# Kernel optimization log

Measured on AMD Instinct MI355X. Metric: run time of the kernel, lower is better.

The kernel has to match this reference:

```python
import jax, jax.numpy as jnp
import numpy as np
import math

B, S, E = 2, 2048, 1024
H, D = 16, 64
LAMBDA_INIT = 0.8
GN_EPS = 1e-5


def setup_inputs() -> dict:
    key = jax.random.key(0)
    ks = jax.random.split(key, 12)
    s = 0.02
    inputs = jax.random.normal(ks[0], (B, S, E), jnp.float32)
    attention_mask = jnp.ones((B, S), jnp.float32)
    token_indices = jnp.sort(jax.random.randint(ks[1], (B, S), 0, S), axis=-1)
    Wq = jax.random.normal(ks[2], (2 * H * D, E), jnp.float32) * s
    Wk = jax.random.normal(ks[3], (2 * H * D, E), jnp.float32) * s
    Wv = jax.random.normal(ks[4], (H * D, E), jnp.float32) * s
    Wo = jax.random.normal(ks[5], (E, H * D), jnp.float32) * s
    lam_q1 = jax.random.normal(ks[6], (D,), jnp.float32) * 0.1
    lam_q2 = jax.random.normal(ks[7], (D,), jnp.float32) * 0.1
    lam_k1 = jax.random.normal(ks[8], (D,), jnp.float32) * 0.1
    lam_k2 = jax.random.normal(ks[9], (D,), jnp.float32) * 0.1
    gn_w = jnp.ones((H * D,), jnp.float32)
    gn_b = jnp.zeros((H * D,), jnp.float32)
    return dict(inputs=inputs, attention_mask=attention_mask, token_indices=token_indices,
                Wq=Wq, Wk=Wk, Wv=Wv, Wo=Wo,
                lam_q1=lam_q1, lam_q2=lam_q2, lam_k1=lam_k1, lam_k2=lam_k2,
                gn_w=gn_w, gn_b=gn_b)


def reference(inputs, attention_mask, token_indices, Wq, Wk, Wv, Wo,
              lam_q1, lam_q2, lam_k1, lam_k2, gn_w, gn_b):
    b, s, e = inputs.shape
    # projections: q,k have doubled head dim (differential), v is standard
    q = (inputs @ Wq.T).reshape(b, s, H, 2 * D).transpose(0, 2, 1, 3)  # [B,H,S,2D]
    k = (inputs @ Wk.T).reshape(b, s, H, 2 * D).transpose(0, 2, 1, 3)
    v = (inputs @ Wv.T).reshape(b, s, H, D).transpose(0, 2, 1, 3)      # [B,H,S,D]
    Q1, Q2 = q[..., :D], q[..., D:]
    K1, K2 = k[..., :D], k[..., D:]
    scale = 1.0 / math.sqrt(D)
    s1 = jnp.einsum('bhqd,bhkd->bhqk', Q1, K1) * scale
    s2 = jnp.einsum('bhqd,bhkd->bhqk', Q2, K2) * scale
    # ALiBi bias: slopes[h] * (pos_q - pos_k), subtracted
    slopes = 2.0 ** (-8.0 * jnp.arange(1, H + 1, dtype=jnp.float32) / H)
    pos = token_indices.astype(jnp.float32)                            # [B,S]
    pos_diff = pos[:, :, None] - pos[:, None, :]                       # [B,S,S]
    bias = slopes[None, :, None, None] * pos_diff[:, None, :, :]       # [B,H,S,S]
    # causal + padding masks
    causal = jnp.triu(jnp.full((s, s), -1e9, jnp.float32), 1)[None, None]
    pad = (1.0 - attention_mask)[:, None, None, :] * -1e9
    s1 = s1 - bias + causal + pad
    s2 = s2 - bias + causal + pad
    w1 = jax.nn.softmax(s1, axis=-1)
    w2 = jax.nn.softmax(s2, axis=-1)
    lam = jnp.exp(jnp.dot(lam_q1, lam_k1)) - jnp.exp(jnp.dot(lam_q2, lam_k2)) + LAMBDA_INIT
    w = w1 - lam * w2
    out = jnp.einsum('bhqk,bhkd->bhqd', w, v)                          # [B,H,S,D]
    # GroupNorm(num_groups=H, num_channels=H*D) over channels-first layout [B,C,S]
    x = out.transpose(0, 2, 1, 3).reshape(b, s, H * D).transpose(0, 2, 1)  # [B,C,S]
    xg = x.reshape(b, H, D * s)
    mean = xg.mean(axis=-1, keepdims=True)
    var = xg.var(axis=-1, keepdims=True)
    xn = ((xg - mean) / jnp.sqrt(var + GN_EPS)).reshape(b, H * D, s)
    xn = xn * gn_w[None, :, None] + gn_b[None, :, None]
    xn = xn * (1.0 - LAMBDA_INIT)
    attn = xn.transpose(0, 2, 1)                                       # [B,S,H*D]
    return attn @ Wo.T
```

## Files before the change

### kernel.cpp

```cpp
#include <hip/hip_runtime.h>
#include <hip/hip_bf16.h>

typedef __hip_bfloat16 bf16;
typedef float f32x4 __attribute__((ext_vector_type(4)));
typedef float fvec4 __attribute__((ext_vector_type(4)));
typedef short s16x8 __attribute__((ext_vector_type(8)));

#define NB_B 2
#define NB_S 2048
#define NB_E 1024
#define NB_H 16
#define NB_D 64

typedef const __attribute__((address_space(1))) void* GPTR;
typedef __attribute__((address_space(3))) void* LPTR;

__device__ __forceinline__ void gld16(const void* g, void* l) {
  __builtin_amdgcn_global_load_lds((GPTR)g, (LPTR)l, 16, 0, 0);
}

__device__ __forceinline__ s16x8 ld8(const bf16* p) { return *(const s16x8*)p; }

__device__ __forceinline__ f32x4 MFMA(s16x8 a, s16x8 b, f32x4 c) {
  return __builtin_amdgcn_mfma_f32_16x16x32_bf16(a, b, c, 0, 0, 0);
}

struct __align__(8) bf16x4 { bf16 a, b, c, d; };

__global__ void cvt_kernel(const float* __restrict__ in, bf16* __restrict__ out, int n4) {
  int i = blockIdx.x * blockDim.x + threadIdx.x;
  if (i >= n4) return;
  fvec4 v = ((const fvec4*)in)[i];
  bf16x4 o = { bf16(v.x), bf16(v.y), bf16(v.z), bf16(v.w) };
  ((bf16x4*)out)[i] = o;
}

__global__ void cvtw_kernel(const float* __restrict__ wq, const float* __restrict__ wk,
                            const float* __restrict__ wv, const float* __restrict__ wo,
                            bf16* __restrict__ oq, bf16* __restrict__ ok,
                            bf16* __restrict__ ov, bf16* __restrict__ oo) {
  int i = blockIdx.x * 256 + threadIdx.x;
  const float* src; bf16* dst; int off;
  if (i < 524288)       { src = wq; dst = oq; off = i; }
  else if (i < 1048576) { src = wk; dst = ok; off = i - 524288; }
  else if (i < 1310720) { src = wv; dst = ov; off = i - 1048576; }
  else                  { src = wo; dst = oo; off = i - 1310720; }
  fvec4 v = ((const fvec4*)src)[off];
  bf16x4 o = { bf16(v.x), bf16(v.y), bf16(v.z), bf16(v.w) };
  ((bf16x4*)dst)[off] = o;
}

__global__ void lam_kernel(const float* lq1, const float* lq2,
                           const float* lk1, const float* lk2, float* out) {
  int l = threadIdx.x;
  float d1 = lq1[l] * lk1[l];
  float d2 = lq2[l] * lk2[l];
#pragma unroll
  for (int o = 32; o; o >>= 1) { d1 += __shfl_xor(d1, o); d2 += __shfl_xor(d2, o); }
  if (l == 0) out[0] = expf(d1) - expf(d2) + 0.8f;
}

__global__ void combo_kernel(const int* __restrict__ tok, const float* __restrict__ amask,
                             float* __restrict__ combo) {
  int i = blockIdx.x * 256 + threadIdx.x;
  int hh = i >> 12, bs = i & 4095;
  float slopeL = exp2f(-0.5f * (float)(hh + 1)) * 1.44269504088896340736f;
  combo[i] = slopeL * (float)tok[bs] + (amask[bs] - 1.f) * 1.44269504e9f;
}

template <int EPI>
__global__ __launch_bounds__(256) void gemm_bt(const bf16* __restrict__ A,
                                               const bf16* __restrict__ Bw,
                                               bf16* __restrict__ Ob,
                                               bf16* __restrict__ Ob2,
                                               bf16* __restrict__ Ob3,
                                               float* __restrict__ Of,
                                               int Kd, float oscale) {
  __shared__ bf16 As[2][128 * 32];
  __shared__ bf16 Bs[2][128 * 32];
  const int tid = threadIdx.x;
  const int lane = tid & 63;
  const int fr = lane & 15, fq = lane >> 4;
  const int wave = tid >> 6;
  const int wr = (wave >> 1) * 64, wc = (wave & 1) * 64;
  const size_t m0 = (size_t)blockIdx.x * 128, n0 = (size_t)blockIdx.y * 128;

  f32x4 acc[4][4];
#pragma unroll
  for (int i = 0; i < 4; i++)
#pragma unroll
    for (int j = 0; j < 4; j++) acc[i][j] = f32x4{0.f, 0.f, 0.f, 0.f};

  const int ca = tid, cb = tid + 256;
  const bf16* ga0 = A + (m0 + (ca >> 2)) * Kd + (ca & 3) * 8;
  const bf16* ga1 = A + (m0 + (cb >> 2)) * Kd + (cb & 3) * 8;
  const bf16* gb0 = Bw + (n0 + (ca >> 2)) * Kd + (ca & 3) * 8;
  const bf16* gb1 = Bw + (n0 + (cb >> 2)) * Kd + (cb & 3) * 8;

  gld16(ga0, &As[0][ca * 8]);
  gld16(ga1, &As[0][cb * 8]);
  gld16(gb0, &Bs[0][ca * 8]);
  gld16(gb1, &Bs[0][cb * 8]);
  __syncthreads();

  const int NKT = Kd >> 5;
  for (int kti = 0; kti < NKT; ++kti) {
    const int cur = kti & 1;
    if (kti + 1 < NKT) {
      const int kt = (kti + 1) << 5;
      gld16(ga0 + kt, &As[cur ^ 1][ca * 8]);
      gld16(ga1 + kt, &As[cur ^ 1][cb * 8]);
      gld16(gb0 + kt, &Bs[cur ^ 1][ca * 8]);
      gld16(gb1 + kt, &Bs[cur ^ 1][cb * 8]);
    }
    s16x8 af[4], bfv[4];
#pragma unroll
    for (int mi = 0; mi < 4; mi++) af[mi] = ld8(&As[cur][(wr + mi * 16 + fr) * 32 + fq * 8]);
#pragma unroll
    for (int ni = 0; ni < 4; ni++) bfv[ni] = ld8(&Bs[cur][(wc + ni * 16 + fr) * 32 + fq * 8]);
#pragma unroll
    for (int mi = 0; mi < 4; mi++)
#pragma unroll
      for (int ni = 0; ni < 4; ni++)
        acc[mi][ni] = MFMA(af[mi], bfv[ni], acc[mi][ni]);
    __syncthreads();
  }

  bf16* dst = Ob;
  size_t nsub = 0;
  float osc = oscale;
  bool isV = false;
  if constexpr (EPI == 0) {
    if (n0 >= 4096)      { dst = Ob3; nsub = 4096; osc = 1.0f; isV = true; }
    else if (n0 >= 2048) { dst = Ob2; nsub = 2048; osc = 1.0f; }
  }

#pragma unroll
  for (int mi = 0; mi < 4; mi++)
#pragma unroll
    for (int ni = 0; ni < 4; ni++)
#pragma unroll
      for (int i = 0; i < 4; i++) {
        size_t m = m0 + wr + mi * 16 + fq * 4 + i;
        size_t n = n0 + wc + ni * 16 + fr;
        if constexpr (EPI == 0) {
          float v = acc[mi][ni][i] * osc;
          size_t nn = n - nsub;
          size_t b = m >> 11, s = m & 2047;
          if (!isV) {
            size_t h = nn >> 7, dd = nn & 127;
            dst[((b * NB_H + h) * NB_S + s) * 128 + dd] = bf16(v);
          } else {
            size_t h = nn >> 6, d = nn & 63;
            dst[((b * NB_H + h) * NB_D + d) * NB_S + s] = bf16(v);
          }
        } else {
          Of[m * 1024 + n] = acc[mi][ni][i] * oscale;
        }
      }
}

__global__ __launch_bounds__(512, 2) void attn_kernel(
    const bf16* __restrict__ Q, const bf16* __restrict__ Kk, const bf16* __restrict__ Vt,
    const int* __restrict__ tok, const float* __restrict__ combo,
    const float* __restrict__ lamp, float* __restrict__ X) {
  __shared__ bf16 Ks[2][2][4096];
  __shared__ bf16 Vs[2][4096];
  __shared__ bf16 Ps[8][1024];

  const int tid = threadIdx.x, lane = tid & 63, wave = tid >> 6;
  const int fr = lane & 15, fq = lane >> 4;
  const int id = blockIdx.x;
  const int w = id >> 3;
  const int bh = (id & 7) * 4 + (w & 3);
  const int qj = 15 - (w >> 2);
  const int b = bh >> 4, h = bh & 15;

  const float lam = lamp[0];
  const float slopeL = exp2f(-0.5f * (float)(h + 1)) * 1.44269504088896340736f;
  const float* comboH = combo + ((size_t)h * NB_B + b) * NB_S;

  const bf16* Kbase = Kk + (size_t)bh * NB_S * 128;
  const bf16* Vbase = Vt + (size_t)bh * NB_D * NB_S;

  const bf16* gK[2]; int lK[2];
#pragma unroll
  for (int i = 0; i < 2; i++) {
    int c = tid + i * 512, set = c >> 9, cc = c & 511;
    int row = cc >> 3, col8 = cc & 7, sc = col8 ^ (row & 7);
    gK[i] = Kbase + (size_t)row * 128 + set * 64 + sc * 8;
    lK[i] = set * 4096 + cc * 8;
  }
  const bf16* gV; int lV;
  {
    int c = tid;
    int row = c >> 3, col8 = c & 7, sc = col8 ^ (row & 7);
    gV = Vbase + (size_t)row * NB_S + sc * 8;
    lV = c * 8;
  }

  const int q0 = qj * 128;
  const int qw = q0 + wave * 16;
  const int ntiles = 2 * qj + 2;

  const bf16* qrow = Q + ((size_t)bh * NB_S + qw + fr) * 128;
  s16x8 q1[2], q2[2];
  q1[0] = ld8(qrow + fq * 8);       q1[1] = ld8(qrow + 32 + fq * 8);
  q2[0] = ld8(qrow + 64 + fq * 8);  q2[1] = ld8(qrow + 96 + fq * 8);

  const int qg = qw + fr;
  const float pq = slopeL * (float)tok[b * NB_S + qg];

  float m1 = -1e30f, m2 = -1e30f, l1 = 0.f, l2 = 0.f;
  f32x4 acc1[4], acc2[4];
#pragma unroll
  for (int nt = 0; nt < 4; nt++) { acc1[nt] = f32x4{0.f,0.f,0.f,0.f}; acc2[nt] = f32x4{0.f,0.f,0.f,0.f}; }

#pragma unroll
  for (int i = 0; i < 2; i++) gld16(gK[i], &Ks[0][0][0] + lK[i]);
  gld16(gV, &Vs[0][0] + lV);
  __syncthreads();

  for (int t = 0; t < ntiles; ++t) {
    const int cur = t & 1;
    const int kv0 = t * 64;
    if (t + 1 < ntiles) {
#pragma unroll
      for (int i = 0; i < 2; i++)
        gld16(gK[i] + (size_t)(kv0 + 64) * 128, &Ks[cur ^ 1][0][0] + lK[i]);
      gld16(gV + (size_t)(kv0 + 64), &Vs[cur ^ 1][0] + lV);
    }

    const bool active = (kv0 <= qw + 15);
    if (active) {
      fvec4 cmbv[4];
#pragma unroll
      for (int nt = 0; nt < 4; nt++)
        cmbv[nt] = *(const fvec4*)(comboH + kv0 + nt * 16 + fq * 4);

      f32x4 c1[4], c2[4];
#pragma unroll
      for (int nt = 0; nt < 4; nt++) { c1[nt] = f32x4{0.f,0.f,0.f,0.f}; c2[nt] = f32x4{0.f,0.f,0.f,0.f}; }
#pragma unroll
      for (int nt = 0; nt < 4; nt++) {
        const int krow = nt * 16 + fr;
#pragma unroll
        for (int kk = 0; kk < 2; kk++) {
          const int sch = ((kk * 4 + fq) ^ (krow & 7)) * 8;
          c1[nt] = MFMA(ld8(&Ks[cur][0][krow * 64 + sch]), q1[kk], c1[nt]);
          c2[nt] = MFMA(ld8(&Ks[cur][1][krow * 64 + sch]), q2[kk], c2[nt]);
        }
      }

      float sv1[4][4], sv2[4][4];
#pragma unroll
      for (int nt = 0; nt < 4; nt++)
#pragma unroll
        for (int i = 0; i < 4; i++) {
          const float biasv = cmbv[nt][i] - pq;
          sv1[nt][i] = c1[nt][i] + biasv;
          sv2[nt][i] = c2[nt][i] + biasv;
        }
      if (kv0 + 63 > qw) {
#pragma unroll
        for (int nt = 0; nt < 4; nt++)
#pragma unroll
          for (int i = 0; i < 4; i++)
            if (kv0 + nt * 16 + fq * 4 + i > qg) { sv1[nt][i] = -1e30f; sv2[nt][i] = -1e30f; }
      }

      s16x8 vf[4][2];
#pragma unroll
      for (int nt = 0; nt < 4; nt++) {
        const int vrow = nt * 16 + fr;
#pragma unroll
        for (int kk = 0; kk < 2; kk++)
          vf[nt][kk] = ld8(&Vs[cur][vrow * 64 + (((kk * 4 + fq) ^ (vrow & 7)) << 3)]);
      }

      {
        float pm = fmaxf(fmaxf(fmaxf(sv1[0][0], sv1[0][1]), fmaxf(sv1[0][2], sv1[0][3])),
                         fmaxf(fmaxf(sv1[1][0], sv1[1][1]), fmaxf(sv1[1][2], sv1[1][3])));
        pm = fmaxf(pm, fmaxf(fmaxf(fmaxf(sv1[2][0], sv1[2][1]), fmaxf(sv1[2][2], sv1[2][3])),
                             fmaxf(fmaxf(sv1[3][0], sv1[3][1]), fmaxf(sv1[3][2], sv1[3][3]))));
        pm = fmaxf(pm, __shfl_xor(pm, 16));
        pm = fmaxf(pm, __shfl_xor(pm, 32));
        if (__any(pm > m1 + 8.f)) {
          const float nm = fmaxf(m1, pm);
          const float cor = exp2f(m1 - nm);
          m1 = nm; l1 *= cor;
#pragma unroll
          for (int i = 0; i < 4; i++) {
            const float ci = __shfl(cor, fq * 4 + i);
#pragma unroll
            for (int nt = 0; nt < 4; nt++) acc1[nt][i] *= ci;
          }
        }
        float rs = 0.f;
#pragma unroll
        for (int nt = 0; nt < 4; nt++) {
          const float p0 = exp2f(sv1[nt][0] - m1), p1 = exp2f(sv1[nt][1] - m1);
          const float p2 = exp2f(sv1[nt][2] - m1), p3 = exp2f(sv1[nt][3] - m1);
          rs += (p0 + p1) + (p2 + p3);
          bf16x4 pk = { bf16(p0), bf16(p1), bf16(p2), bf16(p3) };
          *(bf16x4*)&Ps[wave][fr * 64 + ((((nt * 4 + fq) ^ ((fr & 7) << 1))) << 2)] = pk;
        }
        rs += __shfl_xor(rs, 16);
        rs += __shfl_xor(rs, 32);
        l1 += rs;
#pragma unroll
        for (int kk = 0; kk < 2; kk++) {
          const s16x8 pa = ld8(&Ps[wave][fr * 64 + (((kk * 8 + fq * 2) ^ ((fr & 7) << 1)) << 2)]);
#pragma unroll
          for (int nt = 0; nt < 4; nt++) acc1[nt] = MFMA(pa, vf[nt][kk], acc1[nt]);
        }
      }
      {
        float pm = fmaxf(fmaxf(fmaxf(sv2[0][0], sv2[0][1]), fmaxf(sv2[0][2], sv2[0][3])),
                         fmaxf(fmaxf(sv2[1][0], sv2[1][1]), fmaxf(sv2[1][2], sv2[1][3])));
        pm = fmaxf(pm, fmaxf(fmaxf(fmaxf(sv2[2][0], sv2[2][1]), fmaxf(sv2[2][2], sv2[2][3])),
                             fmaxf(fmaxf(sv2[3][0], sv2[3][1]), fmaxf(sv2[3][2], sv2[3][3]))));
        pm = fmaxf(pm, __shfl_xor(pm, 16));
        pm = fmaxf(pm, __shfl_xor(pm, 32));
        if (__any(pm > m2 + 8.f)) {
          const float nm = fmaxf(m2, pm);
          const float cor = exp2f(m2 - nm);
          m2 = nm; l2 *= cor;
#pragma unroll
          for (int i = 0; i < 4; i++) {
            const float ci = __shfl(cor, fq * 4 + i);
#pragma unroll
            for (int nt = 0; nt < 4; nt++) acc2[nt][i] *= ci;
          }
        }
        float rs = 0.f;
#pragma unroll
        for (int nt = 0; nt < 4; nt++) {
          const float p0 = exp2f(sv2[nt][0] - m2), p1 = exp2f(sv2[nt][1] - m2);
          const float p2 = exp2f(sv2[nt][2] - m2), p3 = exp2f(sv2[nt][3] - m2);
          rs += (p0 + p1) + (p2 + p3);
          bf16x4 pk = { bf16(p0), bf16(p1), bf16(p2), bf16(p3) };
          *(bf16x4*)&Ps[wave][fr * 64 + ((((nt * 4 + fq) ^ ((fr & 7) << 1))) << 2)] = pk;
        }
        rs += __shfl_xor(rs, 16);
        rs += __shfl_xor(rs, 32);
        l2 += rs;
#pragma unroll
        for (int kk = 0; kk < 2; kk++) {
          const s16x8 pa = ld8(&Ps[wave][fr * 64 + (((kk * 8 + fq * 2) ^ ((fr & 7) << 1)) << 2)]);
#pragma unroll
          for (int nt = 0; nt < 4; nt++) acc2[nt] = MFMA(pa, vf[nt][kk], acc2[nt]);
        }
      }
    }

    __syncthreads();
  }

  const float r1 = 1.f / l1, r2 = lam / l2;
  float r1b[4], r2b[4];
#pragma unroll
  for (int i = 0; i < 4; i++) {
    r1b[i] = __shfl(r1, fq * 4 + i);
    r2b[i] = __shfl(r2, fq * 4 + i);
  }
#pragma unroll
  for (int nt = 0; nt < 4; nt++)
#pragma unroll
    for (int i = 0; i < 4; i++) {
      X[((size_t)bh * NB_S + qw + fq * 4 + i) * NB_D + nt * 16 + fr] =
          acc1[nt][i] * r1b[i] - acc2[nt][i] * r2b[i];
    }
}

__global__ __launch_bounds__(256) void gn_part(const float* __restrict__ X, float* __restrict__ part) {
  const int blk = blockIdx.x;
  const int bh = blk >> 3, seg = blk & 7;
  const float* xp = X + (size_t)bh * 131072 + (size_t)seg * 16384;
  float s = 0.f, s2 = 0.f;
  for (int i = threadIdx.x; i < 4096; i += 256) {
    fvec4 v = ((const fvec4*)xp)[i];
    s += v.x + v.y + v.z + v.w;
    s2 += v.x * v.x + v.y * v.y + v.z * v.z + v.w * v.w;
  }
#pragma unroll
  for (int o = 32; o; o >>= 1) { s += __shfl_xor(s, o); s2 += __shfl_xor(s2, o); }
  __shared__ float rs[4], rq[4];
  const int wv = threadIdx.x >> 6, ln = threadIdx.x & 63;
  if (ln == 0) { rs[wv] = s; rq[wv] = s2; }
  __syncthreads();
  if (threadIdx.x == 0) {
    part[blk * 2] = rs[0] + rs[1] + rs[2] + rs[3];
    part[blk * 2 + 1] = rq[0] + rq[1] + rq[2] + rq[3];
  }
}

__global__ __launch_bounds__(256) void gn_apply(const float* __restrict__ X,
                                                const float* __restrict__ part,
                                                const float* __restrict__ gw,
                                                const float* __restrict__ gb,
                                                bf16* __restrict__ Xn) {
  const int blk = blockIdx.x, bh = blk >> 3, seg = blk & 7;
  const int b = bh >> 4, h = bh & 15;
  float s = 0.f, s2 = 0.f;
#pragma unroll
  for (int i = 0; i < 8; i++) { s += part[(bh * 8 + i) * 2]; s2 += part[(bh * 8 + i) * 2 + 1]; }
  const float mean = s * (1.f / 131072.f);
  const float var = s2 * (1.f / 131072.f) - mean * mean;
  const float rstd = rsqrtf(var + 1e-5f) * 0.2f;
  const float* xp = X + (size_t)bh * 131072 + (size_t)seg * 16384;
  for (int i = threadIdx.x; i < 4096; i += 256) {
    fvec4 v = ((const fvec4*)xp)[i];
    const int e = seg * 16384 + i * 4;
    const int srow = e >> 6, d = e & 63;
    const int c = h * 64 + d;
    bf16x4 o = { bf16((v.x - mean) * rstd * gw[c]     + 0.2f * gb[c]),
                 bf16((v.y - mean) * rstd * gw[c + 1] + 0.2f * gb[c + 1]),
                 bf16((v.z - mean) * rstd * gw[c + 2] + 0.2f * gb[c + 2]),
                 bf16((v.w - mean) * rstd * gw[c + 3] + 0.2f * gb[c + 3]) };
    *(bf16x4*)(Xn + ((size_t)b * NB_S + srow) * 1024 + c) = o;
  }
}

extern "C" void kernel_launch(void* const* d_in, const int* in_sizes, int n_in,
                              void* d_out, int out_size, void* d_ws, size_t ws_size,
                              hipStream_t stream) {
  const float* inputs = (const float*)d_in[0];
  const float* amask  = (const float*)d_in[1];
  const int*   tok    = (const int*)d_in[2];
  const float* Wq = (const float*)d_in[3];
  const float* Wk = (const float*)d_in[4];
  const float* Wv = (const float*)d_in[5];
  const float* Wo = (const float*)d_in[6];
  const float* lq1 = (const float*)d_in[7];
  const float* lq2 = (const float*)d_in[8];
  const float* lk1 = (const float*)d_in[9];
  const float* lk2 = (const float*)d_in[10];
  const float* gw = (const float*)d_in[11];
  const float* gb = (const float*)d_in[12];
  float* out = (float*)d_out;
  char* ws = (char*)d_ws;

  bf16* Xbf = (bf16*)(ws + 0);
  bf16* Wqb = (bf16*)(ws + 8388608);
  bf16* Wkb = (bf16*)(ws + 12582912);
  bf16* Wvb = (bf16*)(ws + 16777216);
  float* X  = (float*)(ws + 0);
  float* combo = (float*)(ws + 16777216);
  bf16* Qb  = (bf16*)(ws + 18874368);
  bf16* Xn  = (bf16*)(ws + 18874368);
  bf16* Kb  = (bf16*)(ws + 35651584);
  bf16* Vtb = (bf16*)(ws + 52428800);
  bf16* Wob = (bf16*)(ws + 60817408);
  float* lam = (float*)(ws + 62914560);
  float* gnp = (float*)(ws + 62914816);

  const float QSCALE = 0.125f * 1.44269504088896340736f;

  cvt_kernel<<<4096, 256, 0, stream>>>(inputs, Xbf, 1048576);
  cvtw_kernel<<<6144, 256, 0, stream>>>(Wq, Wk, Wv, Wo, Wqb, Wkb, Wvb, Wob);
  lam_kernel<<<1, 64, 0, stream>>>(lq1, lq2, lk1, lk2, lam);

  gemm_bt<0><<<dim3(32, 40), 256, 0, stream>>>(Xbf, Wqb, Qb, Kb, Vtb, nullptr, 1024, QSCALE);

  combo_kernel<<<256, 256, 0, stream>>>(tok, amask, combo);

  attn_kernel<<<512, 512, 0, stream>>>(Qb, Kb, Vtb, tok, combo, lam, X);

  gn_part<<<256, 256, 0, stream>>>(X, gnp);
  gn_apply<<<256, 256, 0, stream>>>(X, gnp, gw, gb, Xn);

  gemm_bt<2><<<dim3(32, 8), 256, 0, stream>>>(Xn, Wob, nullptr, nullptr, nullptr, out, 1024, 1.0f);
}
```

Baseline: 224.8 us.

## Fuse prep kernels, fold GroupNorm stats into attention, compute row sums via MFMA

Merges the input/weight conversion and lambda kernels into one launch. The attention kernel now writes its output in bf16, accumulates the GroupNorm sum and sum-of-squares with atomics, and drops the separate gn_part pass. Softmax row sums are computed with an extra MFMA against a ones vector instead of shuffles, and s_setprio hints are placed around the MFMA blocks. gn_apply reads bf16 with vectorized 8-wide accesses. This trades some precision (bf16 intermediate, bf16-rounded probabilities used in the row sums) and float atomics for fewer launches and less memory traffic.

```diff
diff --git a/kernel.cpp b/kernel.cpp
--- a/kernel.cpp
+++ b/kernel.cpp
@@ -27,37 +27,41 @@
 
 struct __align__(8) bf16x4 { bf16 a, b, c, d; };
 
-__global__ void cvt_kernel(const float* __restrict__ in, bf16* __restrict__ out, int n4) {
-  int i = blockIdx.x * blockDim.x + threadIdx.x;
-  if (i >= n4) return;
-  fvec4 v = ((const fvec4*)in)[i];
-  bf16x4 o = { bf16(v.x), bf16(v.y), bf16(v.z), bf16(v.w) };
-  ((bf16x4*)out)[i] = o;
-}
-
-__global__ void cvtw_kernel(const float* __restrict__ wq, const float* __restrict__ wk,
+__global__ void prep_kernel(const float* __restrict__ inputs,
+                            const float* __restrict__ wq, const float* __restrict__ wk,
                             const float* __restrict__ wv, const float* __restrict__ wo,
+                            const float* __restrict__ lq1, const float* __restrict__ lq2,
+                            const float* __restrict__ lk1, const float* __restrict__ lk2,
+                            bf16* __restrict__ xbf,
                             bf16* __restrict__ oq, bf16* __restrict__ ok,
-                            bf16* __restrict__ ov, bf16* __restrict__ oo) {
-  int i = blockIdx.x * 256 + threadIdx.x;
-  const float* src; bf16* dst; int off;
-  if (i < 524288)       { src = wq; dst = oq; off = i; }
-  else if (i < 1048576) { src = wk; dst = ok; off = i - 524288; }
-  else if (i < 1310720) { src = wv; dst = ov; off = i - 1048576; }
-  else                  { src = wo; dst = oo; off = i - 1310720; }
-  fvec4 v = ((const fvec4*)src)[off];
-  bf16x4 o = { bf16(v.x), bf16(v.y), bf16(v.z), bf16(v.w) };
-  ((bf16x4*)dst)[off] = o;
-}
-
-__global__ void lam_kernel(const float* lq1, const float* lq2,
-                           const float* lk1, const float* lk2, float* out) {
-  int l = threadIdx.x;
-  float d1 = lq1[l] * lk1[l];
-  float d2 = lq2[l] * lk2[l];
-#pragma unroll
-  for (int o = 32; o; o >>= 1) { d1 += __shfl_xor(d1, o); d2 += __shfl_xor(d2, o); }
-  if (l == 0) out[0] = expf(d1) - expf(d2) + 0.8f;
+                            bf16* __restrict__ ov, bf16* __restrict__ oo,
+                            float* __restrict__ lamo) {
+  const int blk = blockIdx.x;
+  if (blk < 4096) {
+    int i = blk * 256 + threadIdx.x;
+    fvec4 v = ((const fvec4*)inputs)[i];
+    bf16x4 o = { bf16(v.x), bf16(v.y), bf16(v.z), bf16(v.w) };
+    ((bf16x4*)xbf)[i] = o;
+  } else if (blk < 10240) {
+    int i = (blk - 4096) * 256 + threadIdx.x;
+    const float* src; bf16* dst; int off;
+    if (i < 524288)       { src = wq; dst = oq; off = i; }
+    else if (i < 1048576) { src = wk; dst = ok; off = i - 524288; }
+    else if (i < 1310720) { src = wv; dst = ov; off = i - 1048576; }
+    else                  { src = wo; dst = oo; off = i - 1310720; }
+    fvec4 v = ((const fvec4*)src)[off];
+    bf16x4 o = { bf16(v.x), bf16(v.y), bf16(v.z), bf16(v.w) };
+    ((bf16x4*)dst)[off] = o;
+  } else {
+    int l = threadIdx.x;
+    if (l < 64) {
+      float d1 = lq1[l] * lk1[l];
+      float d2 = lq2[l] * lk2[l];
+#pragma unroll
+      for (int o = 32; o; o >>= 1) { d1 += __shfl_xor(d1, o); d2 += __shfl_xor(d2, o); }
+      if (l == 0) lamo[0] = expf(d1) - expf(d2) + 0.8f;
+    }
+  }
 }
 
 __global__ void combo_kernel(const int* __restrict__ tok, const float* __restrict__ amask,
@@ -163,10 +167,11 @@
 __global__ __launch_bounds__(512, 2) void attn_kernel(
     const bf16* __restrict__ Q, const bf16* __restrict__ Kk, const bf16* __restrict__ Vt,
     const int* __restrict__ tok, const float* __restrict__ combo,
-    const float* __restrict__ lamp, float* __restrict__ X) {
+    const float* __restrict__ lamp, bf16* __restrict__ Xb, float* __restrict__ gnp) {
   __shared__ bf16 Ks[2][2][4096];
   __shared__ bf16 Vs[2][4096];
   __shared__ bf16 Ps[8][1024];
+  __shared__ float gs[8][2];
 
   const int tid = threadIdx.x, lane = tid & 63, wave = tid >> 6;
   const int fr = lane & 15, fq = lane >> 4;
@@ -183,6 +188,8 @@
   const bf16* Kbase = Kk + (size_t)bh * NB_S * 128;
   const bf16* Vbase = Vt + (size_t)bh * NB_D * NB_S;
 
+  const s16x8 onesv = { 0x3F80, 0x3F80, 0x3F80, 0x3F80, 0x3F80, 0x3F80, 0x3F80, 0x3F80 };
+
   const bf16* gK[2]; int lK[2];
 #pragma unroll
   for (int i = 0; i < 2; i++) {
@@ -211,8 +218,9 @@
   const int qg = qw + fr;
   const float pq = slopeL * (float)tok[b * NB_S + qg];
 
-  float m1 = -1e30f, m2 = -1e30f, l1 = 0.f, l2 = 0.f;
+  float m1 = -1e30f, m2 = -1e30f;
   f32x4 acc1[4], acc2[4];
+  f32x4 accL1 = f32x4{0.f,0.f,0.f,0.f}, accL2 = f32x4{0.f,0.f,0.f,0.f};
 #pragma unroll
   for (int nt = 0; nt < 4; nt++) { acc1[nt] = f32x4{0.f,0.f,0.f,0.f}; acc2[nt] = f32x4{0.f,0.f,0.f,0.f}; }
 
@@ -241,6 +249,7 @@
       f32x4 c1[4], c2[4];
 #pragma unroll
       for (int nt = 0; nt < 4; nt++) { c1[nt] = f32x4{0.f,0.f,0.f,0.f}; c2[nt] = f32x4{0.f,0.f,0.f,0.f}; }
+      __builtin_amdgcn_s_setprio(1);
 #pragma unroll
       for (int nt = 0; nt < 4; nt++) {
         const int krow = nt * 16 + fr;
@@ -251,6 +260,7 @@
           c2[nt] = MFMA(ld8(&Ks[cur][1][krow * 64 + sch]), q2[kk], c2[nt]);
         }
       }
+      __builtin_amdgcn_s_setprio(0);
 
       float sv1[4][4], sv2[4][4];
 #pragma unroll
@@ -288,32 +298,30 @@
         if (__any(pm > m1 + 8.f)) {
           const float nm = fmaxf(m1, pm);
           const float cor = exp2f(m1 - nm);
-          m1 = nm; l1 *= cor;
+          m1 = nm;
 #pragma unroll
           for (int i = 0; i < 4; i++) {
             const float ci = __shfl(cor, fq * 4 + i);
+            accL1[i] *= ci;
 #pragma unroll
             for (int nt = 0; nt < 4; nt++) acc1[nt][i] *= ci;
           }
         }
-        float rs = 0.f;
 #pragma unroll
         for (int nt = 0; nt < 4; nt++) {
-          const float p0 = exp2f(sv1[nt][0] - m1), p1 = exp2f(sv1[nt][1] - m1);
-          const float p2 = exp2f(sv1[nt][2] - m1), p3 = exp2f(sv1[nt][3] - m1);
-          rs += (p0 + p1) + (p2 + p3);
-          bf16x4 pk = { bf16(p0), bf16(p1), bf16(p2), bf16(p3) };
+          bf16x4 pk = { bf16(exp2f(sv1[nt][0] - m1)), bf16(exp2f(sv1[nt][1] - m1)),
+                        bf16(exp2f(sv1[nt][2] - m1)), bf16(exp2f(sv1[nt][3] - m1)) };
           *(bf16x4*)&Ps[wave][fr * 64 + ((((nt * 4 + fq) ^ ((fr & 7) << 1))) << 2)] = pk;
         }
-        rs += __shfl_xor(rs, 16);
-        rs += __shfl_xor(rs, 32);
-        l1 += rs;
+        __builtin_amdgcn_s_setprio(1);
 #pragma unroll
         for (int kk = 0; kk < 2; kk++) {
           const s16x8 pa = ld8(&Ps[wave][fr * 64 + (((kk * 8 + fq * 2) ^ ((fr & 7) << 1)) << 2)]);
+          accL1 = MFMA(pa, onesv, accL1);
 #pragma unroll
           for (int nt = 0; nt < 4; nt++) acc1[nt] = MFMA(pa, vf[nt][kk], acc1[nt]);
         }
+        __builtin_amdgcn_s_setprio(0);
       }
       {
         float pm = fmaxf(fmaxf(fmaxf(sv2[0][0], sv2[0][1]), fmaxf(sv2[0][2], sv2[0][3])),
@@ -325,100 +333,91 @@
         if (__any(pm > m2 + 8.f)) {
           const float nm = fmaxf(m2, pm);
           const float cor = exp2f(m2 - nm);
-          m2 = nm; l2 *= cor;
+          m2 = nm;
 #pragma unroll
           for (int i = 0; i < 4; i++) {
             const float ci = __shfl(cor, fq * 4 + i);
+            accL2[i] *= ci;
 #pragma unroll
             for (int nt = 0; nt < 4; nt++) acc2[nt][i] *= ci;
           }
         }
-        float rs = 0.f;
 #pragma unroll
         for (int nt = 0; nt < 4; nt++) {
-          const float p0 = exp2f(sv2[nt][0] - m2), p1 = exp2f(sv2[nt][1] - m2);
-          const float p2 = exp2f(sv2[nt][2] - m2), p3 = exp2f(sv2[nt][3] - m2);
-          rs += (p0 + p1) + (p2 + p3);
-          bf16x4 pk = { bf16(p0), bf16(p1), bf16(p2), bf16(p3) };
+          bf16x4 pk = { bf16(exp2f(sv2[nt][0] - m2)), bf16(exp2f(sv2[nt][1] - m2)),
+                        bf16(exp2f(sv2[nt][2] - m2)), bf16(exp2f(sv2[nt][3] - m2)) };
           *(bf16x4*)&Ps[wave][fr * 64 + ((((nt * 4 + fq) ^ ((fr & 7) << 1))) << 2)] = pk;
         }
-        rs += __shfl_xor(rs, 16);
-        rs += __shfl_xor(rs, 32);
-        l2 += rs;
+        __builtin_amdgcn_s_setprio(1);
 #pragma unroll
         for (int kk = 0; kk < 2; kk++) {
           const s16x8 pa = ld8(&Ps[wave][fr * 64 + (((kk * 8 + fq * 2) ^ ((fr & 7) << 1)) << 2)]);
+          accL2 = MFMA(pa, onesv, accL2);
 #pragma unroll
           for (int nt = 0; nt < 4; nt++) acc2[nt] = MFMA(pa, vf[nt][kk], acc2[nt]);
         }
+        __builtin_amdgcn_s_setprio(0);
       }
     }
 
     __syncthreads();
   }
 
-  const float r1 = 1.f / l1, r2 = lam / l2;
   float r1b[4], r2b[4];
 #pragma unroll
-  for (int i = 0; i < 4; i++) {
-    r1b[i] = __shfl(r1, fq * 4 + i);
-    r2b[i] = __shfl(r2, fq * 4 + i);
-  }
+  for (int i = 0; i < 4; i++) { r1b[i] = 1.f / accL1[i]; r2b[i] = lam / accL2[i]; }
+  float s = 0.f, s2 = 0.f;
 #pragma unroll
   for (int nt = 0; nt < 4; nt++)
 #pragma unroll
     for (int i = 0; i < 4; i++) {
-      X[((size_t)bh * NB_S + qw + fq * 4 + i) * NB_D + nt * 16 + fr] =
-          acc1[nt][i] * r1b[i] - acc2[nt][i] * r2b[i];
-    }
-}
-
-__global__ __launch_bounds__(256) void gn_part(const float* __restrict__ X, float* __restrict__ part) {
-  const int blk = blockIdx.x;
-  const int bh = blk >> 3, seg = blk & 7;
-  const float* xp = X + (size_t)bh * 131072 + (size_t)seg * 16384;
-  float s = 0.f, s2 = 0.f;
-  for (int i = threadIdx.x; i < 4096; i += 256) {
-    fvec4 v = ((const fvec4*)xp)[i];
-    s += v.x + v.y + v.z + v.w;
-    s2 += v.x * v.x + v.y * v.y + v.z * v.z + v.w * v.w;
-  }
+      const float v = acc1[nt][i] * r1b[i] - acc2[nt][i] * r2b[i];
+      Xb[((size_t)bh * NB_S + qw + fq * 4 + i) * NB_D + nt * 16 + fr] = bf16(v);
+      s += v; s2 += v * v;
+    }
 #pragma unroll
   for (int o = 32; o; o >>= 1) { s += __shfl_xor(s, o); s2 += __shfl_xor(s2, o); }
-  __shared__ float rs[4], rq[4];
-  const int wv = threadIdx.x >> 6, ln = threadIdx.x & 63;
-  if (ln == 0) { rs[wv] = s; rq[wv] = s2; }
+  if (lane == 0) { gs[wave][0] = s; gs[wave][1] = s2; }
   __syncthreads();
-  if (threadIdx.x == 0) {
-    part[blk * 2] = rs[0] + rs[1] + rs[2] + rs[3];
-    part[blk * 2 + 1] = rq[0] + rq[1] + rq[2] + rq[3];
-  }
-}
-
-__global__ __launch_bounds__(256) void gn_apply(const float* __restrict__ X,
-                                                const float* __restrict__ part,
+  if (tid == 0) {
+    float S = 0.f, S2 = 0.f;
+#pragma unroll
+    for (int i = 0; i < 8; i++) { S += gs[i][0]; S2 += gs[i][1]; }
+    atomicAdd(&gnp[bh * 2], S);
+    atomicAdd(&gnp[bh * 2 + 1], S2);
+  }
+}
+
+__global__ __launch_bounds__(256) void gn_apply(const bf16* __restrict__ Xb,
+                                                const float* __restrict__ gnp,
                                                 const float* __restrict__ gw,
                                                 const float* __restrict__ gb,
                                                 bf16* __restrict__ Xn) {
   const int blk = blockIdx.x, bh = blk >> 3, seg = blk & 7;
   const int b = bh >> 4, h = bh & 15;
-  float s = 0.f, s2 = 0.f;
-#pragma unroll
-  for (int i = 0; i < 8; i++) { s += part[(bh * 8 + i) * 2]; s2 += part[(bh * 8 + i) * 2 + 1]; }
-  const float mean = s * (1.f / 131072.f);
-  const float var = s2 * (1.f / 131072.f) - mean * mean;
+  const float mean = gnp[bh * 2] * (1.f / 131072.f);
+  const float var = gnp[bh * 2 + 1] * (1.f / 131072.f) - mean * mean;
   const float rstd = rsqrtf(var + 1e-5f) * 0.2f;
-  const float* xp = X + (size_t)bh * 131072 + (size_t)seg * 16384;
-  for (int i = threadIdx.x; i < 4096; i += 256) {
-    fvec4 v = ((const fvec4*)xp)[i];
-    const int e = seg * 16384 + i * 4;
-    const int srow = e >> 6, d = e & 63;
-    const int c = h * 64 + d;
-    bf16x4 o = { bf16((v.x - mean) * rstd * gw[c]     + 0.2f * gb[c]),
-                 bf16((v.y - mean) * rstd * gw[c + 1] + 0.2f * gb[c + 1]),
-                 bf16((v.z - mean) * rstd * gw[c + 2] + 0.2f * gb[c + 2]),
-                 bf16((v.w - mean) * rstd * gw[c + 3] + 0.2f * gb[c + 3]) };
-    *(bf16x4*)(Xn + ((size_t)b * NB_S + srow) * 1024 + c) = o;
+  const int tid = threadIdx.x;
+  const int d0 = (tid * 8) & 63;
+  const int c = h * 64 + d0;
+  fvec4 w0 = *(const fvec4*)(gw + c), w1 = *(const fvec4*)(gw + c + 4);
+  fvec4 b0 = *(const fvec4*)(gb + c), b1 = *(const fvec4*)(gb + c + 4);
+  float wv[8] = { w0.x, w0.y, w0.z, w0.w, w1.x, w1.y, w1.z, w1.w };
+  float bv[8] = { b0.x, b0.y, b0.z, b0.w, b1.x, b1.y, b1.z, b1.w };
+  const bf16* xp = Xb + (size_t)bh * 131072;
+#pragma unroll
+  for (int j = 0; j < 8; j++) {
+    const int e = seg * 16384 + (tid + j * 256) * 8;
+    const int srow = e >> 6;
+    s16x8 xv = *(const s16x8*)(xp + e);
+    bf16 o8[8];
+#pragma unroll
+    for (int k = 0; k < 8; k++) {
+      const float xf = __uint_as_float(((unsigned)(unsigned short)xv[k]) << 16);
+      o8[k] = bf16((xf - mean) * rstd * wv[k] + 0.2f * bv[k]);
+    }
+    *(s16x8*)(Xn + ((size_t)b * NB_S + srow) * 1024 + c) = *(const s16x8*)o8;
   }
 }
 
@@ -445,7 +444,7 @@
   bf16* Wqb = (bf16*)(ws + 8388608);
   bf16* Wkb = (bf16*)(ws + 12582912);
   bf16* Wvb = (bf16*)(ws + 16777216);
-  float* X  = (float*)(ws + 0);
+  bf16* Xb  = (bf16*)(ws + 0);
   float* combo = (float*)(ws + 16777216);
   bf16* Qb  = (bf16*)(ws + 18874368);
   bf16* Xn  = (bf16*)(ws + 18874368);
@@ -457,18 +456,17 @@
 
   const float QSCALE = 0.125f * 1.44269504088896340736f;
 
-  cvt_kernel<<<4096, 256, 0, stream>>>(inputs, Xbf, 1048576);
-  cvtw_kernel<<<6144, 256, 0, stream>>>(Wq, Wk, Wv, Wo, Wqb, Wkb, Wvb, Wob);
-  lam_kernel<<<1, 64, 0, stream>>>(lq1, lq2, lk1, lk2, lam);
+  (void)hipMemsetAsync(gnp, 0, 512, stream);
+  prep_kernel<<<10241, 256, 0, stream>>>(inputs, Wq, Wk, Wv, Wo, lq1, lq2, lk1, lk2,
+                                         Xbf, Wqb, Wkb, Wvb, Wob, lam);
 
   gemm_bt<0><<<dim3(32, 40), 256, 0, stream>>>(Xbf, Wqb, Qb, Kb, Vtb, nullptr, 1024, QSCALE);
 
   combo_kernel<<<256, 256, 0, stream>>>(tok, amask, combo);
 
-  attn_kernel<<<512, 512, 0, stream>>>(Qb, Kb, Vtb, tok, combo, lam, X);
-
-  gn_part<<<256, 256, 0, stream>>>(X, gnp);
-  gn_apply<<<256, 256, 0, stream>>>(X, gnp, gw, gb, Xn);
+  attn_kernel<<<512, 512, 0, stream>>>(Qb, Kb, Vtb, tok, combo, lam, Xb, gnp);
+
+  gn_apply<<<256, 256, 0, stream>>>(Xb, gnp, gw, gb, Xn);
 
   gemm_bt<2><<<dim3(32, 8), 256, 0, stream>>>(Xn, Wob, nullptr, nullptr, nullptr, out, 1024, 1.0f);
 }
```

Result: faster. 217.1 us (-3.4%).
